# Kernel tuning notes

Measured on AMD Instinct MI355X. Metric: run time of the kernel, lower is better.

Reference implementation:

```python
import jax, jax.numpy as jnp
import numpy as np
import math

B, H, W, C = 4, 64, 64, 512
G = 32  # GroupNorm groups
EPS = 1e-6


def setup_inputs() -> dict:
    key = jax.random.key(0)
    ks = jax.random.split(key, 6)
    wscale = 1.0 / math.sqrt(C)
    return {
        "x": jax.random.normal(ks[0], (B, H, W, C), jnp.float32),
        "gn_scale": jnp.ones((C,), jnp.float32),
        "gn_bias": jnp.zeros((C,), jnp.float32),
        "wq": jax.random.normal(ks[1], (C, C), jnp.float32) * wscale,
        "bq": jnp.zeros((C,), jnp.float32),
        "wk": jax.random.normal(ks[2], (C, C), jnp.float32) * wscale,
        "bk": jnp.zeros((C,), jnp.float32),
        "wv": jax.random.normal(ks[3], (C, C), jnp.float32) * wscale,
        "bv": jnp.zeros((C,), jnp.float32),
        "wo": jax.random.normal(ks[4], (C, C), jnp.float32) * wscale,
        "bo": jnp.zeros((C,), jnp.float32),
    }


def _group_norm(x, scale, bias):
    # flax nnx.GroupNorm: stats over (H, W, channels-within-group)
    b, h, w, c = x.shape
    xg = x.reshape(b, h, w, G, c // G)
    mean = jnp.mean(xg, axis=(1, 2, 4), keepdims=True)
    var = jnp.mean(jnp.square(xg - mean), axis=(1, 2, 4), keepdims=True)
    xg = (xg - mean) * jax.lax.rsqrt(var + EPS)
    return xg.reshape(b, h, w, c) * scale + bias


def reference(x, gn_scale, gn_bias, wq, bq, wk, bk, wv, bv, wo, bo):
    b, h, w, c = x.shape
    n = h * w
    h_ = _group_norm(x, gn_scale, gn_bias)
    hf = h_.reshape(b, n, c)  # 1x1 conv == per-token matmul
    q = hf @ wq + bq
    k = hf @ wk + bk
    v = hf @ wv + bv
    scale = 1.0 / math.sqrt(c)
    attn = jax.nn.softmax(jnp.einsum('bqc,bkc->bqk', q, k) * scale, axis=-1)
    o = jnp.einsum('bqk,bkc->bqc', attn, v)
    o = o @ wo + bo
    return x + o.reshape(b, h, w, c)
```

## Files before the change

kernel.cpp:

```cpp
#include <hip/hip_runtime.h>
#include <hip/hip_bf16.h>
#include <math.h>


typedef __bf16 bf16;
typedef float f32x4 __attribute__((ext_vector_type(4)));
typedef __bf16 bf16x8 __attribute__((ext_vector_type(8)));
typedef __bf16 bf16x4 __attribute__((ext_vector_type(4)));
typedef long long i64;

#define AS1 __attribute__((address_space(1)))
#define AS3 __attribute__((address_space(3)))

#define NB   4
#define NTOK 4096
#define CCH  512
#define NGRP 32

__device__ __forceinline__ void gload_lds16(const void* g, void* l) {
  __builtin_amdgcn_global_load_lds((AS1 void*)(g), (AS3 void*)(l), 16, 0, 0);
}

__device__ __forceinline__ unsigned char to_e4m3(float f) {
#if __has_builtin(__builtin_amdgcn_cvt_pk_fp8_f32)
  return (unsigned char)(__builtin_amdgcn_cvt_pk_fp8_f32(f, 0.f, 0, false) & 0xff);
#else
  const unsigned u = __float_as_uint(f);
  const unsigned s = (u >> 24) & 0x80;
  const float a = fabsf(f);
  if (a >= 448.f) return (unsigned char)(s | 0x7E);
  if (a < 0.015625f) {
    const int m = (int)rintf(a * 512.f);
    return (unsigned char)(s | m);
  }
  int e = (int)((u >> 23) & 0xff) - 127;
  const float q = exp2f((float)(e - 3));
  int r = (int)rintf(a / q);
  if (r == 16) { e += 1; r = 8; }
  return (unsigned char)(s | ((e + 7) << 3) | (r - 8));
#endif
}

__global__ __launch_bounds__(256) void gn_partial(const float4* __restrict__ x4,
                                                  float* __restrict__ partials) {
  const int chunk = blockIdx.x, b = blockIdx.y;
  const int tid = threadIdx.x;
  const size_t base = ((size_t)b * NTOK + (size_t)chunk * 64) * 128;
  float s = 0.f, ss = 0.f;
  #pragma unroll 4
  for (int it = 0; it < 32; ++it) {
    const float4 v = x4[base + it * 256 + tid];
    s  += v.x + v.y + v.z + v.w;
    ss += v.x * v.x + v.y * v.y + v.z * v.z + v.w * v.w;
  }
  __shared__ float ls[256], lss[256];
  ls[tid] = s; lss[tid] = ss;
  __syncthreads();
  if (tid < 32) {
    float ps = 0.f, pss = 0.f;
    #pragma unroll
    for (int j = 0; j < 4; ++j) {
      ps  += ls[tid * 4 + j] + ls[128 + tid * 4 + j];
      pss += lss[tid * 4 + j] + lss[128 + tid * 4 + j];
    }
    const size_t o = (((size_t)b * 64 + chunk) * 32 + tid) * 2;
    partials[o] = ps; partials[o + 1] = pss;
  }
}

__global__ __launch_bounds__(128) void gn_reduce(const float* __restrict__ partials,
                                                 float* __restrict__ stats) {
  const int tid = threadIdx.x;
  const int b = tid >> 5, g = tid & 31;
  float s = 0.f, ss = 0.f;
  for (int c = 0; c < 64; ++c) {
    const size_t o = (((size_t)b * 64 + c) * 32 + g) * 2;
    s += partials[o]; ss += partials[o + 1];
  }
  const float inv = 1.f / (NTOK * 16.f);
  const float mean = s * inv;
  const float var = ss * inv - mean * mean;
  stats[tid * 2] = mean;
  stats[tid * 2 + 1] = rsqrtf(var + 1e-6f);
}

__global__ __launch_bounds__(256) void gn_apply(const float4* __restrict__ x4,
                                                const float* __restrict__ stats,
                                                const float* __restrict__ gsc,
                                                const float* __restrict__ gbi,
                                                bf16* __restrict__ hf) {
  const int i = blockIdx.x * 256 + threadIdx.x;
  const float4 v = x4[i];
  const size_t e = (size_t)i * 4;
  const int c = (int)(e & (CCH - 1));
  const int b = (int)(e >> 21);
  const int g = c >> 4;
  const float mean = stats[(b * NGRP + g) * 2];
  const float rstd = stats[(b * NGRP + g) * 2 + 1];
  bf16x4 o;
  o[0] = (bf16)((v.x - mean) * rstd * gsc[c + 0] + gbi[c + 0]);
  o[1] = (bf16)((v.y - mean) * rstd * gsc[c + 1] + gbi[c + 1]);
  o[2] = (bf16)((v.z - mean) * rstd * gsc[c + 2] + gbi[c + 2]);
  o[3] = (bf16)((v.w - mean) * rstd * gsc[c + 3] + gbi[c + 3]);
  *reinterpret_cast<bf16x4*>(&hf[e]) = o;
}

__global__ __launch_bounds__(256) void wcast_t(const float* __restrict__ wq,
                                               const float* __restrict__ wk,
                                               const float* __restrict__ bq,
                                               const float* __restrict__ bk,
                                               bf16* __restrict__ dst,
                                               float* __restrict__ bcat) {
  const int w = blockIdx.y;
  const float* src = (w == 0) ? wq : wk;
  bf16* out = dst + (size_t)w * CCH * CCH;
  const int t = blockIdx.x;
  const int tr = t >> 3, tc = t & 7;
  if (t == 0) {
    const float* bsrc = (w == 0) ? bq : bk;
    for (int i = threadIdx.x; i < CCH; i += 256) bcat[w * CCH + i] = bsrc[i];
  }
  __shared__ float tile[64][65];
  for (int i = threadIdx.x; i < 4096; i += 256) {
    const int r = i >> 6, c = i & 63;
    tile[r][c] = src[(size_t)(tr * 64 + r) * CCH + tc * 64 + c];
  }
  __syncthreads();
  for (int i = threadIdx.x; i < 4096; i += 256) {
    const int r = i >> 6, c = i & 63;
    out[(size_t)(tc * 64 + r) * CCH + tr * 64 + c] = (bf16)tile[c][r];
  }
}

__global__ __launch_bounds__(256) void prep_w(const float* __restrict__ wv,
                                              const float* __restrict__ wo,
                                              const float* __restrict__ bv,
                                              const float* __restrict__ bo,
                                              bf16* __restrict__ wpT,
                                              float* __restrict__ bpv) {
  const int ta = blockIdx.x >> 3, tb = blockIdx.x & 7;
  __shared__ float woS[64][65];
  __shared__ float wvS[64][65];
  const int t = threadIdx.x;
  if (blockIdx.x == 0) {
    for (int j = t; j < CCH; j += 256) {
      float a2 = bo[j];
      for (int k2 = 0; k2 < CCH; ++k2) a2 += bv[k2] * wo[(size_t)k2 * CCH + j];
      bpv[j] = a2;
    }
  }
  const int aa0 = (t & 15) * 4, bb0 = (t >> 4) * 4;
  float acc[4][4] = {};
  for (int kt = 0; kt < CCH; kt += 64) {
    for (int i = t; i < 4096; i += 256) {
      const int r = i >> 6, c = i & 63;
      woS[r][c] = wo[(size_t)(kt + r) * CCH + ta * 64 + c];
      wvS[r][c] = wv[(size_t)(tb * 64 + r) * CCH + kt + c];
    }
    __syncthreads();
    #pragma unroll 8
    for (int kk = 0; kk < 64; ++kk) {
      float wo4[4], wv4[4];
      #pragma unroll
      for (int i2 = 0; i2 < 4; ++i2) { wo4[i2] = woS[kk][aa0 + i2]; wv4[i2] = wvS[bb0 + i2][kk]; }
      #pragma unroll
      for (int a2 = 0; a2 < 4; ++a2)
        #pragma unroll
        for (int b2 = 0; b2 < 4; ++b2)
          acc[a2][b2] += wo4[a2] * wv4[b2];
    }
    __syncthreads();
  }
  #pragma unroll
  for (int a2 = 0; a2 < 4; ++a2)
    #pragma unroll
    for (int b2 = 0; b2 < 4; ++b2)
      wpT[(size_t)(ta * 64 + aa0 + a2) * CCH + tb * 64 + bb0 + b2] = (bf16)acc[a2][b2];
}

__global__ __launch_bounds__(256) void rowsum_inv(const float* __restrict__ partials,
                                                  float* __restrict__ rinv) {
  const int row = blockIdx.x * 256 + threadIdx.x;
  const float* p = partials + (size_t)row * 16;
  float s = 0.f;
  #pragma unroll
  for (int j = 0; j < 16; ++j) s += p[j];
  rinv[row] = 1.f / s;
}

template <int BNt, int EPI>
__global__ __launch_bounds__(512, 2) void gemm256(
    const bf16* __restrict__ A, int lda, size_t sA,
    const bf16* __restrict__ Bt, int ldb, size_t sB,
    void* __restrict__ C, int ldc, size_t sC,
    const float* __restrict__ bias,
    float* __restrict__ partials,
    int M, int N, int K, float scale) {
  constexpr int BK = 64;
  constexpr int WN = BNt / 4;
  constexpr int NREP = WN / 16;
  constexpr int BH = BNt / 2;
  constexpr int BISS = BNt / 128;

  __shared__ bf16 Al[2][256 * BK];
  __shared__ bf16 Bl[2][BNt * BK];

  A += (size_t)blockIdx.y * sA;
  Bt += (size_t)blockIdx.y * sB;

  const int tid = threadIdx.x;
  const int lane = tid & 63;
  const int wave = tid >> 6;
  const int wm = wave >> 2, wn = wave & 3;
  const int fr = lane & 15, fq = lane >> 4;
  const int nbn = N / BNt;
  int bm, bn;
  if constexpr (EPI == 4) {
    const int nwg = gridDim.x;
    const int bx = (blockIdx.x & 7) * (nwg >> 3) + (blockIdx.x >> 3);
    bm = bx / nbn; bn = bx % nbn;
  } else {
    const int r = blockIdx.x & 7, q = blockIdx.x >> 3;
    const int pg = q / nbn;
    bm = r + 8 * pg;
    bn = q - pg * nbn;
  }

  const int srow = tid >> 3;
  const int scol = (((tid & 7) ^ (srow & 7)) * 8);
  const bf16* Ab = A + (size_t)(bm * 256 + srow) * lda + scol;
  const bf16* Bb = Bt + (size_t)(bn * BNt + srow) * ldb + scol;

  const int xk = fr & 7;
  const int c0 = ((0 + fq) ^ xk) * 8;
  const int c1 = ((4 + fq) ^ xk) * 8;
  const int aroff = (wm * 128 + fr) * BK;
  const int broff = (wn * WN + fr) * BK;

  f32x4 acc[8][NREP];
  #pragma unroll
  for (int m2 = 0; m2 < 8; ++m2)
    #pragma unroll
    for (int n2 = 0; n2 < NREP; ++n2)
      acc[m2][n2] = f32x4{0.f, 0.f, 0.f, 0.f};
  bf16x8 af[4][2];
  bf16x8 bfr[NREP][2];

#define STAGE_A(buf, h, kt)                                                     \
  { gload_lds16(Ab + (size_t)((h) * 128) * lda + (kt),                          \
                &Al[buf][(h) * 8192 + wave * 512]);                             \
    gload_lds16(Ab + (size_t)((h) * 128 + 64) * lda + (kt),                     \
                &Al[buf][(h) * 8192 + 4096 + wave * 512]); }
#define STAGE_B(buf, h, kt)                                                     \
  { gload_lds16(Bb + (size_t)((h) * BH) * ldb + (kt),                           \
                &Bl[buf][(h) * BH * BK + wave * 512]);                          \
    if (BISS == 2)                                                              \
      gload_lds16(Bb + (size_t)((h) * BH + 64) * ldb + (kt),                    \
                  &Bl[buf][(h) * BH * BK + 4096 + wave * 512]); }
#define LOADA(buf, mh)                                                          \
  { _Pragma("unroll") for (int mi = 0; mi < 4; ++mi) {                          \
      af[mi][0] = *(const bf16x8*)&Al[buf][aroff + ((mh) * 64 + mi * 16) * BK + c0]; \
      af[mi][1] = *(const bf16x8*)&Al[buf][aroff + ((mh) * 64 + mi * 16) * BK + c1]; } }
#define LOADB(buf)                                                              \
  { _Pragma("unroll") for (int ni = 0; ni < NREP; ++ni) {                       \
      bfr[ni][0] = *(const bf16x8*)&Bl[buf][broff + (ni * 16) * BK + c0];       \
      bfr[ni][1] = *(const bf16x8*)&Bl[buf][broff + (ni * 16) * BK + c1]; } }
#define MMA(mh)                                                                 \
  { __builtin_amdgcn_s_setprio(1);                                              \
    _Pragma("unroll") for (int ks = 0; ks < 2; ++ks)                            \
      _Pragma("unroll") for (int mi = 0; mi < 4; ++mi)                          \
        _Pragma("unroll") for (int ni = 0; ni < NREP; ++ni)                     \
          acc[(mh) * 4 + mi][ni] = __builtin_amdgcn_mfma_f32_16x16x32_bf16(     \
              af[mi][ks], bfr[ni][ks], acc[(mh) * 4 + mi][ni], 0, 0, 0);        \
    __builtin_amdgcn_s_setprio(0); }
#define BARX() __builtin_amdgcn_s_barrier()
#define PIN() __builtin_amdgcn_sched_barrier(0)
#define LGKM0() { asm volatile("s_waitcnt lgkmcnt(0)" ::: "memory"); PIN(); }
#define VMW(n) asm volatile("s_waitcnt vmcnt(" #n ")" ::: "memory")
#define VMWSS() { if (BISS == 2) VMW(4); else VMW(3); }

  STAGE_A(0, 0, 0); STAGE_A(0, 1, 0);
  STAGE_B(0, 0, 0); STAGE_B(0, 1, 0);
  STAGE_A(1, 0, BK); STAGE_B(1, 0, BK);
  VMWSS();
  BARX();

  const int niter = K >> 7;
  for (int j = 0; j < niter; ++j) {
    const int kt1 = j * 128 + 64;
    const int kt2 = kt1 + 64, kt3 = kt1 + 128;
    const bool last = (j == niter - 1);
    LOADA(0, 0); LOADB(0); STAGE_A(1, 1, kt1); STAGE_B(1, 1, kt1);
    PIN(); BARX(); LGKM0(); MMA(0); BARX();
    LOADA(0, 1); if (!last) { STAGE_A(0, 0, kt2); STAGE_B(0, 0, kt2); }
    PIN(); BARX(); LGKM0(); MMA(1);
    if (last) { VMW(0); } else VMWSS();
    BARX();
    LOADA(1, 0); LOADB(1); if (!last) { STAGE_A(0, 1, kt2); STAGE_B(0, 1, kt2); }
    PIN(); BARX(); LGKM0(); MMA(0); BARX();
    LOADA(1, 1); if (!last) { STAGE_A(1, 0, kt3); STAGE_B(1, 0, kt3); }
    PIN(); BARX(); LGKM0(); MMA(1);
    if (!last) VMWSS();
    BARX();
  }

  const int crow0 = bm * 256 + wm * 128 + fq * 4;
  const int ccol0 = bn * BNt + wn * WN + fr;
  if constexpr (EPI == 1) {
    float* sums = (float*)&Al[0][0];
    #pragma unroll
    for (int mh = 0; mh < 2; ++mh)
      #pragma unroll
      for (int mi = 0; mi < 4; ++mi)
        #pragma unroll
        for (int jj = 0; jj < 4; ++jj) {
          const int row = crow0 + mh * 64 + mi * 16 + jj;
          float rs = 0.f;
          #pragma unroll
          for (int nr = 0; nr < NREP; ++nr) {
            const float e = __expf(fminf(acc[mh * 4 + mi][nr][jj], 6.10f));
            rs += e;
            ((unsigned char*)C)[(size_t)blockIdx.y * sC + (size_t)row * ldc + ccol0 + nr * 16] = to_e4m3(e);
          }
          rs += __shfl_xor(rs, 1); rs += __shfl_xor(rs, 2);
          rs += __shfl_xor(rs, 4); rs += __shfl_xor(rs, 8);
          if (fr == 0)
            sums[(wm * 128 + mh * 64 + mi * 16 + fq * 4 + jj) * 4 + wn] = rs;
        }
    __syncthreads();
    if (tid < 256) {
      const float s4 = sums[tid * 4] + sums[tid * 4 + 1] +
                       sums[tid * 4 + 2] + sums[tid * 4 + 3];
      partials[((size_t)blockIdx.y * M + bm * 256 + tid) * (size_t)nbn + bn] = s4;
    }
  } else {
    #pragma unroll
    for (int mh = 0; mh < 2; ++mh)
      #pragma unroll
      for (int mi = 0; mi < 4; ++mi)
        #pragma unroll
        for (int nr = 0; nr < NREP; ++nr)
          #pragma unroll
          for (int jj = 0; jj < 4; ++jj) {
            const int row = crow0 + mh * 64 + mi * 16 + jj;
            const int col = ccol0 + nr * 16;
            const float val = acc[mh * 4 + mi][nr][jj];
            const size_t idx = (size_t)row * ldc + col;
            if constexpr (EPI == 0) {
              float vv = val + bias[col];
              if (col < CCH) vv *= scale;
              ((bf16*)C)[(size_t)blockIdx.y * sC + idx] = (bf16)vv;
            } else {
              ((unsigned char*)C)[(size_t)blockIdx.y * sC + idx] = to_e4m3(val);
            }
          }
  }
#undef STAGE_A
#undef STAGE_B
#undef LOADA
#undef LOADB
#undef MMA
#undef BARX
#undef PIN
#undef LGKM0
#undef VMW
#undef VMWSS
}

__global__ __launch_bounds__(512, 2) void pv_fp8(
    const unsigned char* __restrict__ S8,
    const unsigned char* __restrict__ V8,
    float* __restrict__ out, const float* __restrict__ bpv,
    const float* __restrict__ x, const float* __restrict__ rinv, int vofs) {
  __shared__ unsigned char Sl[2][16384];
  __shared__ unsigned char Vl[2][8192];
  const int bb = blockIdx.y;
  const unsigned char* A8 = S8 + (size_t)bb * NTOK * NTOK;
  const int tid = threadIdx.x, lane = tid & 63, wave = tid >> 6;
  const int wm = wave >> 2, wn = wave & 3;
  const int fr = lane & 15, fq = lane >> 4;
  const int r_ = blockIdx.x & 7, q_ = blockIdx.x >> 3;
  const int pg = q_ >> 2;
  const int bm = r_ + 8 * pg, bn = q_ & 3;

  const int sr = tid >> 2;
  const int aswz = ((tid & 3) ^ ((tid >> 3) & 3)) * 16;
  const unsigned char* Ab = A8 + (size_t)(bm * 256 + sr) * NTOK + aswz;
  const unsigned char* Bb = V8 + (size_t)(bn * 128 + sr) * (NB * NTOK)
                            + vofs + bb * NTOK + aswz;

  const int xA = fr & 6;
  const int c0 = (fq ^ xA) * 8;
  const int c1 = ((fq ^ 4) ^ xA) * 8;

  f32x4 acc[8][2];
  #pragma unroll
  for (int m2 = 0; m2 < 8; ++m2)
    #pragma unroll
    for (int n2 = 0; n2 < 2; ++n2)
      acc[m2][n2] = f32x4{0.f, 0.f, 0.f, 0.f};
  i64 af8[4][2], bf8[2][2];

#define PSTAGE_A(buf, kt)                                                       \
  { gload_lds16(Ab + (kt), (char*)&Sl[buf][0] + tid * 16);                      \
    gload_lds16(Ab + (size_t)128 * NTOK + (kt), (char*)&Sl[buf][0] + 8192 + tid * 16); }
#define PSTAGE_B(buf, kt)                                                       \
  gload_lds16(Bb + (kt), (char*)&Vl[buf][0] + tid * 16);
#define PLOADA(buf, mh)                                                         \
  { _Pragma("unroll") for (int mi = 0; mi < 4; ++mi) {                          \
      const int ro = (wm * 128 + (mh) * 64 + mi * 16 + fr) * 64;                \
      af8[mi][0] = *(const i64*)&Sl[buf][ro + c0];                              \
      af8[mi][1] = *(const i64*)&Sl[buf][ro + c1]; } }
#define PLOADB(buf)                                                             \
  { _Pragma("unroll") for (int ni = 0; ni < 2; ++ni) {                          \
      const int ro = (wn * 32 + ni * 16 + fr) * 64;                             \
      bf8[ni][0] = *(const i64*)&Vl[buf][ro + c0];                              \
      bf8[ni][1] = *(const i64*)&Vl[buf][ro + c1]; } }
#define PMMA(mh)                                                                \
  { __builtin_amdgcn_s_setprio(1);                                              \
    _Pragma("unroll") for (int ks = 0; ks < 2; ++ks)                            \
      _Pragma("unroll") for (int mi = 0; mi < 4; ++mi)                          \
        _Pragma("unroll") for (int ni = 0; ni < 2; ++ni)                        \
          acc[(mh) * 4 + mi][ni] = __builtin_amdgcn_mfma_f32_16x16x32_fp8_fp8(  \
              af8[mi][ks], bf8[ni][ks], acc[(mh) * 4 + mi][ni], 0, 0, 0);       \
    __builtin_amdgcn_s_setprio(0); }
#define PBARX() __builtin_amdgcn_s_barrier()
#define PPIN() __builtin_amdgcn_sched_barrier(0)
#define PLGKM0() { asm volatile("s_waitcnt lgkmcnt(0)" ::: "memory"); PPIN(); }
#define PVMW(n) asm volatile("s_waitcnt vmcnt(" #n ")" ::: "memory")

  PSTAGE_B(0, 0); PSTAGE_A(0, 0); PSTAGE_B(1, 64);
  PVMW(1);
  PBARX();

  const int niter = 32;
  for (int j = 0; j < niter; ++j) {
    const int kt0 = j * 128;
    const bool last = (j == niter - 1);
    PLOADA(0, 0); PLOADB(0); PSTAGE_A(1, kt0 + 64);
    PPIN(); PBARX(); PLGKM0(); PMMA(0); PBARX();
    PLOADA(0, 1); if (!last) PSTAGE_B(0, kt0 + 128);
    PPIN(); PBARX(); PLGKM0(); PMMA(1);
    if (last) { PVMW(0); } else { PVMW(1); }
    PBARX();
    PLOADA(1, 0); PLOADB(1); if (!last) PSTAGE_A(0, kt0 + 128);
    PPIN(); PBARX(); PLGKM0(); PMMA(0); PBARX();
    PLOADA(1, 1); if (!last) PSTAGE_B(1, kt0 + 192);
    PPIN(); PBARX(); PLGKM0(); PMMA(1);
    if (last) { PVMW(0); } else { PVMW(1); }
    PBARX();
  }

  const int crow0 = bm * 256 + wm * 128 + fq * 4;
  const int ccol0 = bn * 128 + wn * 32 + fr;
  #pragma unroll
  for (int mh = 0; mh < 2; ++mh)
    #pragma unroll
    for (int mi = 0; mi < 4; ++mi)
      #pragma unroll
      for (int jj = 0; jj < 4; ++jj) {
        const int row = crow0 + mh * 64 + mi * 16 + jj;
        const float ri = rinv[(size_t)bb * NTOK + row];
        #pragma unroll
        for (int ni = 0; ni < 2; ++ni) {
          const int col = ccol0 + ni * 16;
          const size_t idx = ((size_t)bb * NTOK + row) * CCH + col;
          out[idx] = acc[mh * 4 + mi][ni][jj] * ri + bpv[col] + x[idx];
        }
      }
#undef PSTAGE_A
#undef PSTAGE_B
#undef PLOADA
#undef PLOADB
#undef PMMA
#undef PBARX
#undef PPIN
#undef PLGKM0
#undef PVMW
}

extern "C" void kernel_launch(void* const* d_in, const int* in_sizes, int n_in,
                              void* d_out, int out_size, void* d_ws, size_t ws_size,
                              hipStream_t stream) {
  const float* x   = (const float*)d_in[0];
  const float* gsc = (const float*)d_in[1];
  const float* gbi = (const float*)d_in[2];
  const float* wq  = (const float*)d_in[3];
  const float* bq  = (const float*)d_in[4];
  const float* wk  = (const float*)d_in[5];
  const float* bk  = (const float*)d_in[6];
  const float* wv  = (const float*)d_in[7];
  const float* bv  = (const float*)d_in[8];
  const float* wo  = (const float*)d_in[9];
  const float* bo  = (const float*)d_in[10];
  float* out = (float*)d_out;
  char* ws = (char*)d_ws;

  const float sscale = 0.044194173824159216f;
  const bool batched = ws_size >= 111810560ULL;

  if (batched) {
    unsigned char* S8  = (unsigned char*)(ws + 0);
    bf16*  hf    = (bf16*)(ws + 0);
    bf16*  qk    = (bf16*)(ws + 67108864);
    unsigned char* vt8 = (unsigned char*)(ws + 100663296);
    bf16*  wT    = (bf16*)(ws + 109051904);
    float* bcat  = (float*)(ws + 110624768);
    float* bpv   = (float*)(ws + 110628864);
    float* stats = (float*)(ws + 110630912);
    float* parts = (float*)(ws + 110631936);
    float* spart = (float*)(ws + 110695936);
    float* rinv  = (float*)(ws + 111744512);

    gn_partial<<<dim3(64, NB), 256, 0, stream>>>((const float4*)x, parts);
    gn_reduce<<<1, 128, 0, stream>>>(parts, stats);
    gn_apply<<<8192, 256, 0, stream>>>((const float4*)x, stats, gsc, gbi, hf);
    wcast_t<<<dim3(64, 2), 256, 0, stream>>>(wq, wk, bq, bk, wT, bcat);
    prep_w<<<64, 256, 0, stream>>>(wv, wo, bv, bo, wT + 2 * CCH * CCH, bpv);

    gemm256<128, 0><<<dim3(512, 1), 512, 0, stream>>>(
        hf, 512, 0, wT, 512, 0, qk, 1024, 0, bcat, nullptr,
        16384, 1024, 512, sscale);
    gemm256<128, 4><<<dim3(256, 1), 512, 0, stream>>>(
        wT + 2 * CCH * CCH, 512, 0, hf, 512, 0, vt8, 16384, 0,
        nullptr, nullptr, 512, 16384, 512, 0.f);
    gemm256<256, 1><<<dim3(256, NB), 512, 0, stream>>>(
        qk, 1024, (size_t)NTOK * 1024, qk + 512, 1024, (size_t)NTOK * 1024,
        S8, NTOK, (size_t)NTOK * NTOK, nullptr, spart,
        NTOK, NTOK, CCH, 0.f);
    rowsum_inv<<<64, 256, 0, stream>>>(spart, rinv);
    pv_fp8<<<dim3(64, NB), 512, 0, stream>>>(S8, vt8, out, bpv, x, rinv, 0);
  } else {
    unsigned char* S81 = (unsigned char*)(ws + 0);
    bf16*  hf    = (bf16*)(ws + 0);
    bf16*  qk    = (bf16*)(ws + 16777216);
    unsigned char* vt8 = (unsigned char*)(ws + 50331648);
    bf16*  wT    = (bf16*)(ws + 58720256);
    float* bcat  = (float*)(ws + 60293120);
    float* bpv   = (float*)(ws + 60297216);
    float* stats = (float*)(ws + 60299264);
    float* parts = (float*)(ws + 60300288);
    float* spart = (float*)(ws + 60364800);
    float* rinv  = (float*)(ws + 60620800);

    gn_partial<<<dim3(64, NB), 256, 0, stream>>>((const float4*)x, parts);
    gn_reduce<<<1, 128, 0, stream>>>(parts, stats);
    gn_apply<<<8192, 256, 0, stream>>>((const float4*)x, stats, gsc, gbi, hf);
    wcast_t<<<dim3(64, 2), 256, 0, stream>>>(wq, wk, bq, bk, wT, bcat);
    prep_w<<<64, 256, 0, stream>>>(wv, wo, bv, bo, wT + 2 * CCH * CCH, bpv);
    gemm256<128, 0><<<dim3(512, 1), 512, 0, stream>>>(
        hf, 512, 0, wT, 512, 0, qk, 1024, 0, bcat, nullptr,
        16384, 1024, 512, sscale);
    gemm256<128, 4><<<dim3(256, 1), 512, 0, stream>>>(
        wT + 2 * CCH * CCH, 512, 0, hf, 512, 0, vt8, 16384, 0,
        nullptr, nullptr, 512, 16384, 512, 0.f);
    for (int b = 0; b < NB; ++b) {
      const bf16* qb = qk + (size_t)b * NTOK * 1024;
      gemm256<256, 1><<<dim3(256, 1), 512, 0, stream>>>(
          qb, 1024, 0, qb + 512, 1024, 0, S81, NTOK, 0, nullptr, spart,
          NTOK, NTOK, CCH, 0.f);
      rowsum_inv<<<16, 256, 0, stream>>>(spart, rinv);
      pv_fp8<<<dim3(64, 1), 512, 0, stream>>>(
          S81, vt8, out + (size_t)b * NTOK * CCH, bpv,
          x + (size_t)b * NTOK * CCH, rinv, b * NTOK);
    }
  }
}
```

Measured before the change: 309.4 us.

## Store Q/K in fp8 and compute attention scores with fp8 MFMA kernel

The QK projection GEMM now writes Q and K as fp8 e4m3 instead of bf16, with the softmax scale moved into the scores epilogue. A new scores_fp8 kernel uses fp8 MFMA with 256x128 tiles, halving the bytes loaded per score and increasing occupancy, and writes 32 partial row sums per row instead of 16. This cuts memory traffic and raises MFMA throughput for the QK^T stage, at the cost of extra precision loss in Q and K and more, smaller blocks.

```diff
diff --git a/kernel.cpp b/kernel.cpp
--- a/kernel.cpp
+++ b/kernel.cpp
@@ -181,32 +181,27 @@
 __global__ __launch_bounds__(256) void rowsum_inv(const float* __restrict__ partials,
                                                   float* __restrict__ rinv) {
   const int row = blockIdx.x * 256 + threadIdx.x;
-  const float* p = partials + (size_t)row * 16;
+  const float* p = partials + (size_t)row * 32;
   float s = 0.f;
   #pragma unroll
-  for (int j = 0; j < 16; ++j) s += p[j];
+  for (int j = 0; j < 32; ++j) s += p[j];
   rinv[row] = 1.f / s;
 }
 
-template <int BNt, int EPI>
+template <int EPI>
 __global__ __launch_bounds__(512, 2) void gemm256(
-    const bf16* __restrict__ A, int lda, size_t sA,
-    const bf16* __restrict__ Bt, int ldb, size_t sB,
-    void* __restrict__ C, int ldc, size_t sC,
+    const bf16* __restrict__ A, int lda,
+    const bf16* __restrict__ Bt, int ldb,
+    unsigned char* __restrict__ C, int ldc,
     const float* __restrict__ bias,
-    float* __restrict__ partials,
-    int M, int N, int K, float scale) {
+    int M, int N, int K) {
   constexpr int BK = 64;
-  constexpr int WN = BNt / 4;
-  constexpr int NREP = WN / 16;
-  constexpr int BH = BNt / 2;
-  constexpr int BISS = BNt / 128;
+  constexpr int BNt = 128;
+  constexpr int WN = 32;
+  constexpr int NREP = 2;
 
   __shared__ bf16 Al[2][256 * BK];
   __shared__ bf16 Bl[2][BNt * BK];
-
-  A += (size_t)blockIdx.y * sA;
-  Bt += (size_t)blockIdx.y * sB;
 
   const int tid = threadIdx.x;
   const int lane = tid & 63;
@@ -252,11 +247,8 @@
     gload_lds16(Ab + (size_t)((h) * 128 + 64) * lda + (kt),                     \
                 &Al[buf][(h) * 8192 + 4096 + wave * 512]); }
 #define STAGE_B(buf, h, kt)                                                     \
-  { gload_lds16(Bb + (size_t)((h) * BH) * ldb + (kt),                           \
-                &Bl[buf][(h) * BH * BK + wave * 512]);                          \
-    if (BISS == 2)                                                              \
-      gload_lds16(Bb + (size_t)((h) * BH + 64) * ldb + (kt),                    \
-                  &Bl[buf][(h) * BH * BK + 4096 + wave * 512]); }
+  gload_lds16(Bb + (size_t)((h) * 64) * ldb + (kt),                             \
+              &Bl[buf][(h) * 4096 + wave * 512]);
 #define LOADA(buf, mh)                                                          \
   { _Pragma("unroll") for (int mi = 0; mi < 4; ++mi) {                          \
       af[mi][0] = *(const bf16x8*)&Al[buf][aroff + ((mh) * 64 + mi * 16) * BK + c0]; \
@@ -277,12 +269,11 @@
 #define PIN() __builtin_amdgcn_sched_barrier(0)
 #define LGKM0() { asm volatile("s_waitcnt lgkmcnt(0)" ::: "memory"); PIN(); }
 #define VMW(n) asm volatile("s_waitcnt vmcnt(" #n ")" ::: "memory")
-#define VMWSS() { if (BISS == 2) VMW(4); else VMW(3); }
 
   STAGE_A(0, 0, 0); STAGE_A(0, 1, 0);
   STAGE_B(0, 0, 0); STAGE_B(0, 1, 0);
   STAGE_A(1, 0, BK); STAGE_B(1, 0, BK);
-  VMWSS();
+  VMW(3);
   BARX();
 
   const int niter = K >> 7;
@@ -294,67 +285,36 @@
     PIN(); BARX(); LGKM0(); MMA(0); BARX();
     LOADA(0, 1); if (!last) { STAGE_A(0, 0, kt2); STAGE_B(0, 0, kt2); }
     PIN(); BARX(); LGKM0(); MMA(1);
-    if (last) { VMW(0); } else VMWSS();
+    if (last) { VMW(0); } else VMW(3);
     BARX();
     LOADA(1, 0); LOADB(1); if (!last) { STAGE_A(0, 1, kt2); STAGE_B(0, 1, kt2); }
     PIN(); BARX(); LGKM0(); MMA(0); BARX();
     LOADA(1, 1); if (!last) { STAGE_A(1, 0, kt3); STAGE_B(1, 0, kt3); }
     PIN(); BARX(); LGKM0(); MMA(1);
-    if (!last) VMWSS();
+    if (!last) VMW(3);
     BARX();
   }
 
   const int crow0 = bm * 256 + wm * 128 + fq * 4;
   const int ccol0 = bn * BNt + wn * WN + fr;
-  if constexpr (EPI == 1) {
-    float* sums = (float*)&Al[0][0];
-    #pragma unroll
-    for (int mh = 0; mh < 2; ++mh)
+  #pragma unroll
+  for (int mh = 0; mh < 2; ++mh)
+    #pragma unroll
+    for (int mi = 0; mi < 4; ++mi)
       #pragma unroll
-      for (int mi = 0; mi < 4; ++mi)
+      for (int nr = 0; nr < NREP; ++nr)
         #pragma unroll
         for (int jj = 0; jj < 4; ++jj) {
           const int row = crow0 + mh * 64 + mi * 16 + jj;
-          float rs = 0.f;
-          #pragma unroll
-          for (int nr = 0; nr < NREP; ++nr) {
-            const float e = __expf(fminf(acc[mh * 4 + mi][nr][jj], 6.10f));
-            rs += e;
-            ((unsigned char*)C)[(size_t)blockIdx.y * sC + (size_t)row * ldc + ccol0 + nr * 16] = to_e4m3(e);
+          const int col = ccol0 + nr * 16;
+          const float val = acc[mh * 4 + mi][nr][jj];
+          const size_t idx = (size_t)row * ldc + col;
+          if constexpr (EPI == 0) {
+            C[idx] = to_e4m3(val + bias[col]);
+          } else {
+            C[idx] = to_e4m3(val);
           }
-          rs += __shfl_xor(rs, 1); rs += __shfl_xor(rs, 2);
-          rs += __shfl_xor(rs, 4); rs += __shfl_xor(rs, 8);
-          if (fr == 0)
-            sums[(wm * 128 + mh * 64 + mi * 16 + fq * 4 + jj) * 4 + wn] = rs;
         }
-    __syncthreads();
-    if (tid < 256) {
-      const float s4 = sums[tid * 4] + sums[tid * 4 + 1] +
-                       sums[tid * 4 + 2] + sums[tid * 4 + 3];
-      partials[((size_t)blockIdx.y * M + bm * 256 + tid) * (size_t)nbn + bn] = s4;
-    }
-  } else {
-    #pragma unroll
-    for (int mh = 0; mh < 2; ++mh)
-      #pragma unroll
-      for (int mi = 0; mi < 4; ++mi)
-        #pragma unroll
-        for (int nr = 0; nr < NREP; ++nr)
-          #pragma unroll
-          for (int jj = 0; jj < 4; ++jj) {
-            const int row = crow0 + mh * 64 + mi * 16 + jj;
-            const int col = ccol0 + nr * 16;
-            const float val = acc[mh * 4 + mi][nr][jj];
-            const size_t idx = (size_t)row * ldc + col;
-            if constexpr (EPI == 0) {
-              float vv = val + bias[col];
-              if (col < CCH) vv *= scale;
-              ((bf16*)C)[(size_t)blockIdx.y * sC + idx] = (bf16)vv;
-            } else {
-              ((unsigned char*)C)[(size_t)blockIdx.y * sC + idx] = to_e4m3(val);
-            }
-          }
-  }
 #undef STAGE_A
 #undef STAGE_B
 #undef LOADA
@@ -364,7 +324,129 @@
 #undef PIN
 #undef LGKM0
 #undef VMW
-#undef VMWSS
+}
+
+__global__ __launch_bounds__(512, 4) void scores_fp8(
+    const unsigned char* __restrict__ qk,
+    unsigned char* __restrict__ S8,
+    float* __restrict__ partials,
+    float sscale) {
+  __shared__ unsigned char Ql[2][16384];
+  __shared__ unsigned char Kl[2][8192];
+  const int bb = blockIdx.y;
+  const unsigned char* Aq = qk + (size_t)bb * NTOK * 1024;
+  const int tid = threadIdx.x, lane = tid & 63, wave = tid >> 6;
+  const int wm = wave >> 2, wn = wave & 3;
+  const int fr = lane & 15, fq = lane >> 4;
+  const int r_ = blockIdx.x & 7, q_ = blockIdx.x >> 3;
+  const int pg = q_ >> 5;
+  const int bm = r_ + 8 * pg, bn = q_ & 31;
+
+  const int sr = tid >> 2;
+  const int aswz = ((tid & 3) ^ ((tid >> 3) & 3)) * 16;
+  const unsigned char* Ab = Aq + (size_t)(bm * 256 + sr) * 1024 + aswz;
+  const unsigned char* Bb = Aq + (size_t)(bn * 128 + sr) * 1024 + 512 + aswz;
+
+  const int xA = fr & 6;
+  const int c0 = (fq ^ xA) * 8;
+  const int c1 = ((fq ^ 4) ^ xA) * 8;
+
+  f32x4 acc[8][2];
+  #pragma unroll
+  for (int m2 = 0; m2 < 8; ++m2)
+    #pragma unroll
+    for (int n2 = 0; n2 < 2; ++n2)
+      acc[m2][n2] = f32x4{0.f, 0.f, 0.f, 0.f};
+  i64 af8[4][2], bf8[2][2];
+
+#define SSTAGE_A(buf, kt)                                                       \
+  { gload_lds16(Ab + (kt), (char*)&Ql[buf][0] + tid * 16);                      \
+    gload_lds16(Ab + (size_t)128 * 1024 + (kt), (char*)&Ql[buf][0] + 8192 + tid * 16); }
+#define SSTAGE_B(buf, kt)                                                       \
+  gload_lds16(Bb + (kt), (char*)&Kl[buf][0] + tid * 16);
+#define SLOADA(buf, mh)                                                         \
+  { _Pragma("unroll") for (int mi = 0; mi < 4; ++mi) {                          \
+      const int ro = (wm * 128 + (mh) * 64 + mi * 16 + fr) * 64;                \
+      af8[mi][0] = *(const i64*)&Ql[buf][ro + c0];                              \
+      af8[mi][1] = *(const i64*)&Ql[buf][ro + c1]; } }
+#define SLOADB(buf)                                                             \
+  { _Pragma("unroll") for (int ni = 0; ni < 2; ++ni) {                          \
+      const int ro = (wn * 32 + ni * 16 + fr) * 64;                             \
+      bf8[ni][0] = *(const i64*)&Kl[buf][ro + c0];                              \
+      bf8[ni][1] = *(const i64*)&Kl[buf][ro + c1]; } }
+#define SMMA(mh)                                                                \
+  { __builtin_amdgcn_s_setprio(1);                                              \
+    _Pragma("unroll") for (int ks = 0; ks < 2; ++ks)                            \
+      _Pragma("unroll") for (int mi = 0; mi < 4; ++mi)                          \
+        _Pragma("unroll") for (int ni = 0; ni < 2; ++ni)                        \
+          acc[(mh) * 4 + mi][ni] = __builtin_amdgcn_mfma_f32_16x16x32_fp8_fp8(  \
+              af8[mi][ks], bf8[ni][ks], acc[(mh) * 4 + mi][ni], 0, 0, 0);       \
+    __builtin_amdgcn_s_setprio(0); }
+#define SBARX() __builtin_amdgcn_s_barrier()
+#define SPIN() __builtin_amdgcn_sched_barrier(0)
+#define SLGKM0() { asm volatile("s_waitcnt lgkmcnt(0)" ::: "memory"); SPIN(); }
+#define SVMW(n) asm volatile("s_waitcnt vmcnt(" #n ")" ::: "memory")
+
+  SSTAGE_B(0, 0); SSTAGE_A(0, 0); SSTAGE_B(1, 64);
+  SVMW(1);
+  SBARX();
+
+  const int niter = 4;
+  for (int j = 0; j < niter; ++j) {
+    const int kt0 = j * 128;
+    const bool last = (j == niter - 1);
+    SLOADA(0, 0); SLOADB(0); SSTAGE_A(1, kt0 + 64);
+    SPIN(); SBARX(); SLGKM0(); SMMA(0); SBARX();
+    SLOADA(0, 1); if (!last) SSTAGE_B(0, kt0 + 128);
+    SPIN(); SBARX(); SLGKM0(); SMMA(1);
+    if (last) { SVMW(0); } else { SVMW(1); }
+    SBARX();
+    SLOADA(1, 0); SLOADB(1); if (!last) SSTAGE_A(0, kt0 + 128);
+    SPIN(); SBARX(); SLGKM0(); SMMA(0); SBARX();
+    SLOADA(1, 1); if (!last) SSTAGE_B(1, kt0 + 192);
+    SPIN(); SBARX(); SLGKM0(); SMMA(1);
+    if (last) { SVMW(0); } else { SVMW(1); }
+    SBARX();
+  }
+
+  unsigned char* Cb = S8 + (size_t)bb * NTOK * NTOK;
+  const int crow0 = bm * 256 + wm * 128 + fq * 4;
+  const int ccol0 = bn * 128 + wn * 32 + fr;
+  float* sums = (float*)&Ql[0][0];
+  #pragma unroll
+  for (int mh = 0; mh < 2; ++mh)
+    #pragma unroll
+    for (int mi = 0; mi < 4; ++mi)
+      #pragma unroll
+      for (int jj = 0; jj < 4; ++jj) {
+        const int row = crow0 + mh * 64 + mi * 16 + jj;
+        float rs = 0.f;
+        #pragma unroll
+        for (int ni = 0; ni < 2; ++ni) {
+          const float e = __expf(fminf(acc[mh * 4 + mi][ni][jj] * sscale, 6.10f));
+          rs += e;
+          Cb[(size_t)row * NTOK + ccol0 + ni * 16] = to_e4m3(e);
+        }
+        rs += __shfl_xor(rs, 1); rs += __shfl_xor(rs, 2);
+        rs += __shfl_xor(rs, 4); rs += __shfl_xor(rs, 8);
+        if (fr == 0)
+          sums[(wm * 128 + mh * 64 + mi * 16 + fq * 4 + jj) * 4 + wn] = rs;
+      }
+  __syncthreads();
+  if (tid < 256) {
+    const float s4 = sums[tid * 4] + sums[tid * 4 + 1] +
+                     sums[tid * 4 + 2] + sums[tid * 4 + 3];
+    partials[((size_t)bb * NTOK + bm * 256 + tid) * 32 + bn] = s4;
+  }
+#undef SSTAGE_A
+#undef SSTAGE_B
+#undef SLOADA
+#undef SLOADB
+#undef SMMA
+#undef SBARX
+#undef SPIN
+#undef SLGKM0
+#undef SVMW
 }
 
 __global__ __launch_bounds__(512, 2) void pv_fp8(
@@ -497,20 +579,20 @@
   char* ws = (char*)d_ws;
 
   const float sscale = 0.044194173824159216f;
-  const bool batched = ws_size >= 111810560ULL;
+  const bool batched = ws_size >= 96082944ULL;
 
   if (batched) {
     unsigned char* S8  = (unsigned char*)(ws + 0);
     bf16*  hf    = (bf16*)(ws + 0);
-    bf16*  qk    = (bf16*)(ws + 67108864);
-    unsigned char* vt8 = (unsigned char*)(ws + 100663296);
-    bf16*  wT    = (bf16*)(ws + 109051904);
-    float* bcat  = (float*)(ws + 110624768);
-    float* bpv   = (float*)(ws + 110628864);
-    float* stats = (float*)(ws + 110630912);
-    float* parts = (float*)(ws + 110631936);
-    float* spart = (float*)(ws + 110695936);
-    float* rinv  = (float*)(ws + 111744512);
+    unsigned char* qk8 = (unsigned char*)(ws + 67108864);
+    unsigned char* vt8 = (unsigned char*)(ws + 83886080);
+    bf16*  wT    = (bf16*)(ws + 92274688);
+    float* bcat  = (float*)(ws + 93847552);
+    float* bpv   = (float*)(ws + 93851648);
+    float* stats = (float*)(ws + 93853696);
+    float* parts = (float*)(ws + 93854720);
+    float* spart = (float*)(ws + 93920256);
+    float* rinv  = (float*)(ws + 96017408);
 
     gn_partial<<<dim3(64, NB), 256, 0, stream>>>((const float4*)x, parts);
     gn_reduce<<<1, 128, 0, stream>>>(parts, stats);
@@ -518,47 +600,38 @@
     wcast_t<<<dim3(64, 2), 256, 0, stream>>>(wq, wk, bq, bk, wT, bcat);
     prep_w<<<64, 256, 0, stream>>>(wv, wo, bv, bo, wT + 2 * CCH * CCH, bpv);
 
-    gemm256<128, 0><<<dim3(512, 1), 512, 0, stream>>>(
-        hf, 512, 0, wT, 512, 0, qk, 1024, 0, bcat, nullptr,
-        16384, 1024, 512, sscale);
-    gemm256<128, 4><<<dim3(256, 1), 512, 0, stream>>>(
-        wT + 2 * CCH * CCH, 512, 0, hf, 512, 0, vt8, 16384, 0,
-        nullptr, nullptr, 512, 16384, 512, 0.f);
-    gemm256<256, 1><<<dim3(256, NB), 512, 0, stream>>>(
-        qk, 1024, (size_t)NTOK * 1024, qk + 512, 1024, (size_t)NTOK * 1024,
-        S8, NTOK, (size_t)NTOK * NTOK, nullptr, spart,
-        NTOK, NTOK, CCH, 0.f);
+    gemm256<0><<<dim3(512, 1), 512, 0, stream>>>(
+        hf, 512, wT, 512, qk8, 1024, bcat, 16384, 1024, 512);
+    gemm256<4><<<dim3(256, 1), 512, 0, stream>>>(
+        wT + 2 * CCH * CCH, 512, hf, 512, vt8, 16384, nullptr, 512, 16384, 512);
+    scores_fp8<<<dim3(512, NB), 512, 0, stream>>>(qk8, S8, spart, sscale);
     rowsum_inv<<<64, 256, 0, stream>>>(spart, rinv);
     pv_fp8<<<dim3(64, NB), 512, 0, stream>>>(S8, vt8, out, bpv, x, rinv, 0);
   } else {
     unsigned char* S81 = (unsigned char*)(ws + 0);
     bf16*  hf    = (bf16*)(ws + 0);
-    bf16*  qk    = (bf16*)(ws + 16777216);
-    unsigned char* vt8 = (unsigned char*)(ws + 50331648);
-    bf16*  wT    = (bf16*)(ws + 58720256);
-    float* bcat  = (float*)(ws + 60293120);
-    float* bpv   = (float*)(ws + 60297216);
-    float* stats = (float*)(ws + 60299264);
-    float* parts = (float*)(ws + 60300288);
-    float* spart = (float*)(ws + 60364800);
-    float* rinv  = (float*)(ws + 60620800);
+    unsigned char* qk8 = (unsigned char*)(ws + 16777216);
+    unsigned char* vt8 = (unsigned char*)(ws + 33554432);
+    bf16*  wT    = (bf16*)(ws + 41943040);
+    float* bcat  = (float*)(ws + 43515904);
+    float* bpv   = (float*)(ws + 43520000);
+    float* stats = (float*)(ws + 43522048);
+    float* parts = (float*)(ws + 43523072);
+    float* spart = (float*)(ws + 43588608);
+    float* rinv  = (float*)(ws + 44112896);
 
     gn_partial<<<dim3(64, NB), 256, 0, stream>>>((const float4*)x, parts);
     gn_reduce<<<1, 128, 0, stream>>>(parts, stats);
     gn_apply<<<8192, 256, 0, stream>>>((const float4*)x, stats, gsc, gbi, hf);
     wcast_t<<<dim3(64, 2), 256, 0, stream>>>(wq, wk, bq, bk, wT, bcat);
     prep_w<<<64, 256, 0, stream>>>(wv, wo, bv, bo, wT + 2 * CCH * CCH, bpv);
-    gemm256<128, 0><<<dim3(512, 1), 512, 0, stream>>>(
-        hf, 512, 0, wT, 512, 0, qk, 1024, 0, bcat, nullptr,
-        16384, 1024, 512, sscale);
-    gemm256<128, 4><<<dim3(256, 1), 512, 0, stream>>>(
-        wT + 2 * CCH * CCH, 512, 0, hf, 512, 0, vt8, 16384, 0,
-        nullptr, nullptr, 512, 16384, 512, 0.f);
+    gemm256<0><<<dim3(512, 1), 512, 0, stream>>>(
+        hf, 512, wT, 512, qk8, 1024, bcat, 16384, 1024, 512);
+    gemm256<4><<<dim3(256, 1), 512, 0, stream>>>(
+        wT + 2 * CCH * CCH, 512, hf, 512, vt8, 16384, nullptr, 512, 16384, 512);
     for (int b = 0; b < NB; ++b) {
-      const bf16* qb = qk + (size_t)b * NTOK * 1024;
-      gemm256<256, 1><<<dim3(256, 1), 512, 0, stream>>>(
-          qb, 1024, 0, qb + 512, 1024, 0, S81, NTOK, 0, nullptr, spart,
-          NTOK, NTOK, CCH, 0.f);
+      scores_fp8<<<dim3(512, 1), 512, 0, stream>>>(
+          qk8 + (size_t)b * NTOK * 1024, S81, spart, sscale);
       rowsum_inv<<<16, 256, 0, stream>>>(spart, rinv);
       pv_fp8<<<dim3(64, 1), 512, 0, stream>>>(
           S81, vt8, out + (size_t)b * NTOK * CCH, bpv,
```

After: 288.8 us. 1.07x faster.
